# Kernel optimization log

Hardware: AMD Instinct MI355X
Metric: run time of the kernel (lower is better)

The kernel has to match this reference:

```python
import jax, jax.numpy as jnp
import numpy as np

B, C, W, H, K = 8, 512, 64, 64, 64
C4 = C // 4

def setup_inputs() -> dict:
    key = jax.random.key(0)
    ks = jax.random.split(key, 12)
    return {
        "x1": jax.random.normal(ks[0], (B, C, W, H), jnp.float32),
        "y1": jax.random.normal(ks[1], (B, K, C), jnp.float32),
        "x2": jax.random.normal(ks[2], (B, C, W, H), jnp.float32),
        "y2": jax.random.normal(ks[3], (B, K, C), jnp.float32),
        "wq": jax.random.normal(ks[4], (C4, C), jnp.float32) * 0.02,
        "bq": jax.random.normal(ks[5], (C4,), jnp.float32) * 0.02,
        "wk": jax.random.normal(ks[6], (C4, C), jnp.float32) * 0.02,
        "bk": jax.random.normal(ks[7], (C4,), jnp.float32) * 0.02,
        "wv": jax.random.normal(ks[8], (C, C), jnp.float32) * 0.02,
        "bv": jax.random.normal(ks[9], (C,), jnp.float32) * 0.02,
        "scale": jax.random.normal(ks[10], (1,), jnp.float32),
        "scale1": jax.random.normal(ks[11], (1,), jnp.float32),
    }

def reference(x1, y1, x2, y2, wq, bq, wk, bk, wv, bv, scale, scale1):
    b, c, w, h = x1.shape
    k = y1.shape[1]
    n = w * h
    # value projections (nn.Linear: y @ W^T + b), kept as [B, C, K]
    pv1 = jnp.einsum('bkc,dc->bdk', y1, wv) + bv[None, :, None]
    pv2 = jnp.einsum('bkc,dc->bdk', y2, wv) + bv[None, :, None]
    # 1x1 conv query: [B, C4, W, H] -> [B, N, C4]
    q = jnp.einsum('bcwh,dc->bwhd', x2, wq) + bq
    q = q.reshape(b, n, -1)
    # key: [B, K, C4] -> bmm contracts over C4
    kk = jnp.einsum('bkc,dc->bkd', y2, wk) + bk  # [B, K, C4]
    energy = jnp.einsum('bnd,bkd->bnk', q, kk)   # [B, N, K]
    attention = jax.nn.softmax(jnp.abs(energy), axis=-1)
    # out = value [B,C,K] @ attention^T [B,K,N] -> [B,C,N]
    out1 = jnp.einsum('bck,bnk->bcn', pv1, attention).reshape(b, c, w, h)
    out1 = scale[0] * out1 + x1
    out2 = jnp.einsum('bck,bnk->bcn', pv2, attention).reshape(b, c, w, h)
    out2 = scale1[0] * out2 + x2
    return (out1, out2)
```

## Files before the change

### kernel.cpp

```cpp
#include <hip/hip_runtime.h>
#include <math.h>

#define Bn 8
#define Cn 512
#define Kn 64
#define C4n 128
#define Nn 4096

typedef short bf16x8 __attribute__((ext_vector_type(8)));
typedef float f32x4  __attribute__((ext_vector_type(4)));
typedef unsigned short u16;

__device__ __forceinline__ u16 f2bf(float f) {
    union { float f; unsigned u; } v; v.f = f;
    unsigned r = v.u + 0x7FFF + ((v.u >> 16) & 1);
    return (u16)(r >> 16);
}
__device__ __forceinline__ float bf2f(u16 h) {
    union { unsigned u; float f; } v; v.u = ((unsigned)h) << 16;
    return v.f;
}
__device__ __forceinline__ bf16x8 cvt8(const float* p) {
    float4 a = *(const float4*)p;
    float4 b = *(const float4*)(p + 4);
    bf16x8 r;
    r[0] = (short)f2bf(a.x); r[1] = (short)f2bf(a.y);
    r[2] = (short)f2bf(a.z); r[3] = (short)f2bf(a.w);
    r[4] = (short)f2bf(b.x); r[5] = (short)f2bf(b.y);
    r[6] = (short)f2bf(b.z); r[7] = (short)f2bf(b.w);
    return r;
}

__global__ __launch_bounds__(256) void kk_pv_kernel(
    const float* __restrict__ y1, const float* __restrict__ y2,
    const float* __restrict__ wv, const float* __restrict__ bv,
    const float* __restrict__ wk, const float* __restrict__ bk,
    u16* __restrict__ pv1h, u16* __restrict__ pv2h, u16* __restrict__ kkh)
{
    const int b    = blockIdx.y;
    const int sel  = blockIdx.z;
    const int lane = threadIdx.x & 63;
    const int wid  = threadIdx.x >> 6;
    const int lr   = lane & 15;
    const int lg   = lane >> 4;

    if (sel < 2) {
        const int cb   = blockIdx.x * 64 + wid * 16;
        const float* y = sel ? y2 : y1;
        u16* pvh       = sel ? pv2h : pv1h;

        f32x4 acc[4];
        #pragma unroll
        for (int kt = 0; kt < 4; ++kt) acc[kt] = (f32x4){0.f, 0.f, 0.f, 0.f};

        for (int c0 = 0; c0 < Cn; c0 += 32) {
            const int cf = c0 + lg * 8;
            bf16x8 wfr = cvt8(wv + (size_t)(cb + lr) * Cn + cf);
            bf16x8 yfr[4];
            #pragma unroll
            for (int kt = 0; kt < 4; ++kt)
                yfr[kt] = cvt8(y + (size_t)(b * Kn + kt * 16 + lr) * Cn + cf);
            #pragma unroll
            for (int kt = 0; kt < 4; ++kt)
                acc[kt] = __builtin_amdgcn_mfma_f32_16x16x32_bf16(
                    yfr[kt], wfr, acc[kt], 0, 0, 0);
        }
        const int c = cb + lr;
        const float bb = bv[c];
        #pragma unroll
        for (int kt = 0; kt < 4; ++kt) {
            ushort4 o;
            o.x = f2bf(acc[kt][0] + bb); o.y = f2bf(acc[kt][1] + bb);
            o.z = f2bf(acc[kt][2] + bb); o.w = f2bf(acc[kt][3] + bb);
            *(ushort4*)&pvh[(((size_t)(b * Cn + c)) << 6) + kt * 16 + 4 * lg] = o;
        }
    } else {
        const int dblk = blockIdx.x * 16;
        f32x4 acc = (f32x4){0.f, 0.f, 0.f, 0.f};
        for (int c0 = 0; c0 < Cn; c0 += 32) {
            const int cf = c0 + lg * 8;
            bf16x8 wfr = cvt8(wk + (size_t)(dblk + lr) * Cn + cf);
            bf16x8 yfr = cvt8(y2 + (size_t)(b * Kn + wid * 16 + lr) * Cn + cf);
            acc = __builtin_amdgcn_mfma_f32_16x16x32_bf16(wfr, yfr, acc, 0, 0, 0);
        }
        const int d4 = dblk + 4 * lg;
        float4 bkv = *(const float4*)&bk[d4];
        ushort4 o;
        o.x = f2bf(acc[0] + bkv.x); o.y = f2bf(acc[1] + bkv.y);
        o.z = f2bf(acc[2] + bkv.z); o.w = f2bf(acc[3] + bkv.w);
        *(ushort4*)&kkh[(((size_t)(b * Kn + wid * 16 + lr)) << 7) + d4] = o;
    }
}

__global__ __launch_bounds__(256) void M_e0_kernel(
    const u16* __restrict__ kkh, const float* __restrict__ wq,
    const float* __restrict__ bq, u16* __restrict__ Mth,
    float* __restrict__ e0)
{
    const int b = blockIdx.y;
    const int t = threadIdx.x;

    if (blockIdx.x == 4) {
        if (t < Kn) {
            const u16* row = kkh + (((size_t)(b * Kn + t)) << 7);
            float acc = 0.f;
            #pragma unroll
            for (int d8 = 0; d8 < C4n; d8 += 8) {
                bf16x8 v = *(const bf16x8*)(row + d8);
                #pragma unroll
                for (int j = 0; j < 8; ++j)
                    acc += bq[d8 + j] * bf2f((u16)v[j]);
            }
            e0[b * Kn + t] = acc;
        }
        return;
    }

    const int cb   = blockIdx.x * 128 + (t >> 6) * 32;
    const int lane = t & 63;
    const int lr   = lane & 15;
    const int lg   = lane >> 4;

    f32x4 acc[2][4];
    #pragma unroll
    for (int ct = 0; ct < 2; ++ct)
        #pragma unroll
        for (int kt = 0; kt < 4; ++kt) acc[ct][kt] = (f32x4){0.f, 0.f, 0.f, 0.f};

    for (int d0 = 0; d0 < C4n; d0 += 32) {
        const int df = d0 + lg * 8;
        bf16x8 afr[2];
        #pragma unroll
        for (int ct = 0; ct < 2; ++ct) {
            const int c = cb + ct * 16 + lr;
            bf16x8 r;
            #pragma unroll
            for (int j = 0; j < 8; ++j)
                r[j] = (short)f2bf(wq[(size_t)(df + j) * Cn + c]);
            afr[ct] = r;
        }
        bf16x8 bfr[4];
        #pragma unroll
        for (int kt = 0; kt < 4; ++kt)
            bfr[kt] = *(const bf16x8*)&kkh[(((size_t)(b * Kn + kt * 16 + lr)) << 7) + df];
        #pragma unroll
        for (int ct = 0; ct < 2; ++ct)
            #pragma unroll
            for (int kt = 0; kt < 4; ++kt)
                acc[ct][kt] = __builtin_amdgcn_mfma_f32_16x16x32_bf16(
                    afr[ct], bfr[kt], acc[ct][kt], 0, 0, 0);
    }
    #pragma unroll
    for (int ct = 0; ct < 2; ++ct) {
        const int c4 = cb + ct * 16 + 4 * lg;
        #pragma unroll
        for (int kt = 0; kt < 4; ++kt) {
            ushort4 o;
            o.x = f2bf(acc[ct][kt][0]); o.y = f2bf(acc[ct][kt][1]);
            o.z = f2bf(acc[ct][kt][2]); o.w = f2bf(acc[ct][kt][3]);
            *(ushort4*)&Mth[(size_t)(b * Kn + kt * 16 + lr) * Cn + c4] = o;
        }
    }
}

__global__ __launch_bounds__(256) void attn_out_kernel(
    const float* __restrict__ x1, const float* __restrict__ x2,
    const u16* __restrict__ pv1h, const u16* __restrict__ pv2h,
    const u16* __restrict__ Mth, const float* __restrict__ e0,
    const float* __restrict__ scale, const float* __restrict__ scale1,
    float* __restrict__ out1, float* __restrict__ out2)
{
    __shared__ u16   attL[64 * 64];
    __shared__ float T[4][16 * 68];

    const int id   = blockIdx.x;
    const int b    = id & 7;
    const int n0   = (id >> 3) * 64;
    const int t    = threadIdx.x;
    const int lane = t & 63;
    const int wid  = t >> 6;
    const int lr   = lane & 15;
    const int lg   = lane >> 4;
    const int nl   = wid * 16 + lr;

    f32x4 eacc[4];
    #pragma unroll
    for (int kt = 0; kt < 4; ++kt) eacc[kt] = (f32x4){0.f, 0.f, 0.f, 0.f};

    const float* xcol = x2 + (((size_t)b * Cn) << 12) + n0 + nl;
    const u16*   mb   = Mth + ((size_t)b << 15) + (size_t)lr * Cn;

    for (int c0 = 0; c0 < Cn; c0 += 32) {
        const int cf = c0 + lg * 8;
        float xs[8];
        #pragma unroll
        for (int j = 0; j < 8; ++j)
            xs[j] = xcol[((size_t)(cf + j)) << 12];
        bf16x8 xfr;
        #pragma unroll
        for (int j = 0; j < 8; ++j) xfr[j] = (short)f2bf(xs[j]);
        #pragma unroll
        for (int kt = 0; kt < 4; ++kt) {
            bf16x8 av = *(const bf16x8*)(mb + ((size_t)kt << 13) + cf);
            eacc[kt] = __builtin_amdgcn_mfma_f32_16x16x32_bf16(av, xfr, eacc[kt], 0, 0, 0);
        }
    }

    {
        float a[4][4];
        float mx = 0.f;
        #pragma unroll
        for (int kt = 0; kt < 4; ++kt) {
            float4 e0v = *(const float4*)&e0[b * Kn + kt * 16 + lg * 4];
            float er[4] = {e0v.x, e0v.y, e0v.z, e0v.w};
            #pragma unroll
            for (int reg = 0; reg < 4; ++reg) {
                float v = fabsf(eacc[kt][reg] + er[reg]);
                a[kt][reg] = v;
                mx = fmaxf(mx, v);
            }
        }
        mx = fmaxf(mx, __shfl_xor(mx, 16));
        mx = fmaxf(mx, __shfl_xor(mx, 32));
        float s = 0.f;
        #pragma unroll
        for (int kt = 0; kt < 4; ++kt)
            #pragma unroll
            for (int reg = 0; reg < 4; ++reg) {
                a[kt][reg] = __expf(a[kt][reg] - mx);
                s += a[kt][reg];
            }
        s += __shfl_xor(s, 16);
        s += __shfl_xor(s, 32);
        const float inv = 1.0f / s;

        #pragma unroll
        for (int kt = 0; kt < 4; ++kt) {
            ushort4 o;
            o.x = f2bf(a[kt][0] * inv); o.y = f2bf(a[kt][1] * inv);
            o.z = f2bf(a[kt][2] * inv); o.w = f2bf(a[kt][3] * inv);
            const int chunk = (kt * 2 + (lg >> 1)) ^ (nl & 7);
            *(ushort4*)&attL[nl * 64 + chunk * 8 + 4 * (lg & 1)] = o;
        }
    }
    __syncthreads();

    bf16x8 af[4][2];
    #pragma unroll
    for (int nt = 0; nt < 4; ++nt)
        #pragma unroll
        for (int ks = 0; ks < 2; ++ks) {
            const int nn = nt * 16 + lr;
            const int chunk = (ks * 4 + lg) ^ (nn & 7);
            af[nt][ks] = *(const bf16x8*)&attL[nn * 64 + chunk * 8];
        }

    const float sA = scale[0], sB = scale1[0];
    float* Tw = &T[wid][0];

    for (int ct = 0; ct < 8; ++ct) {
        const int wc = ct * 64 + wid * 16;

        const u16* p1 = pv1h + (((size_t)(b * Cn + wc + lr)) << 6) + lg * 8;
        const u16* p2 = pv2h + (((size_t)(b * Cn + wc + lr)) << 6) + lg * 8;
        bf16x8 v1[2], v2[2];
        v1[0] = *(const bf16x8*)p1;  v1[1] = *(const bf16x8*)(p1 + 32);
        v2[0] = *(const bf16x8*)p2;  v2[1] = *(const bf16x8*)(p2 + 32);

        f32x4 acc1[4], acc2[4];
        #pragma unroll
        for (int nt = 0; nt < 4; ++nt) {
            f32x4 z = (f32x4){0.f, 0.f, 0.f, 0.f};
            acc1[nt] = __builtin_amdgcn_mfma_f32_16x16x32_bf16(af[nt][0], v1[0], z, 0, 0, 0);
            acc1[nt] = __builtin_amdgcn_mfma_f32_16x16x32_bf16(af[nt][1], v1[1], acc1[nt], 0, 0, 0);
            acc2[nt] = __builtin_amdgcn_mfma_f32_16x16x32_bf16(af[nt][0], v2[0], z, 0, 0, 0);
            acc2[nt] = __builtin_amdgcn_mfma_f32_16x16x32_bf16(af[nt][1], v2[1], acc2[nt], 0, 0, 0);
        }

        #pragma unroll
        for (int nt = 0; nt < 4; ++nt) {
            float4 v;
            v.x = acc1[nt][0]; v.y = acc1[nt][1];
            v.z = acc1[nt][2]; v.w = acc1[nt][3];
            *(float4*)&Tw[lr * 68 + nt * 16 + 4 * lg] = v;
        }
        #pragma unroll
        for (int r4 = 0; r4 < 4; ++r4) {
            const int rloc = r4 * 4 + lg;
            const size_t row = (((size_t)(b * Cn + wc + rloc)) << 12) + n0 + lr * 4;
            float4 a = *(const float4*)&Tw[rloc * 68 + lr * 4];
            float4 xv = *(const float4*)&x1[row];
            f32x4 o;
            o[0] = sA * a.x + xv.x;  o[1] = sA * a.y + xv.y;
            o[2] = sA * a.z + xv.z;  o[3] = sA * a.w + xv.w;
            __builtin_nontemporal_store(o, (f32x4*)&out1[row]);
        }

        #pragma unroll
        for (int nt = 0; nt < 4; ++nt) {
            float4 v;
            v.x = acc2[nt][0]; v.y = acc2[nt][1];
            v.z = acc2[nt][2]; v.w = acc2[nt][3];
            *(float4*)&Tw[lr * 68 + nt * 16 + 4 * lg] = v;
        }
        #pragma unroll
        for (int r4 = 0; r4 < 4; ++r4) {
            const int rloc = r4 * 4 + lg;
            const size_t row = (((size_t)(b * Cn + wc + rloc)) << 12) + n0 + lr * 4;
            float4 a = *(const float4*)&Tw[rloc * 68 + lr * 4];
            float4 xv = *(const float4*)&x2[row];
            f32x4 o;
            o[0] = sB * a.x + xv.x;  o[1] = sB * a.y + xv.y;
            o[2] = sB * a.z + xv.z;  o[3] = sB * a.w + xv.w;
            __builtin_nontemporal_store(o, (f32x4*)&out2[row]);
        }
    }
}

extern "C" void kernel_launch(void* const* d_in, const int* in_sizes, int n_in,
                              void* d_out, int out_size, void* d_ws, size_t ws_size,
                              hipStream_t stream)
{
    const float* x1     = (const float*)d_in[0];
    const float* y1     = (const float*)d_in[1];
    const float* x2     = (const float*)d_in[2];
    const float* y2     = (const float*)d_in[3];
    const float* wq     = (const float*)d_in[4];
    const float* bq     = (const float*)d_in[5];
    const float* wk     = (const float*)d_in[6];
    const float* bk     = (const float*)d_in[7];
    const float* wv     = (const float*)d_in[8];
    const float* bv     = (const float*)d_in[9];
    const float* scale  = (const float*)d_in[10];
    const float* scale1 = (const float*)d_in[11];

    float* out1 = (float*)d_out;
    float* out2 = out1 + (size_t)Bn * Cn * Nn;

    float* ws   = (float*)d_ws;
    float* e0   = ws;
    u16*   kkh  = (u16*)(ws + 512);
    u16*   Mth  = kkh + 65536;
    u16*   pv1h = Mth + 262144;
    u16*   pv2h = pv1h + 262144;

    kk_pv_kernel<<<dim3(8, Bn, 3), 256, 0, stream>>>(
        y1, y2, wv, bv, wk, bk, pv1h, pv2h, kkh);
    M_e0_kernel<<<dim3(5, Bn), 256, 0, stream>>>(kkh, wq, bq, Mth, e0);
    attn_out_kernel<<<512, 256, 0, stream>>>(
        x1, x2, pv1h, pv2h, Mth, e0, scale, scale1, out1, out2);
}
```

Baseline: 86.04 us.

## Software-pipeline value and residual loads in attention output loop

In the output loop, the pv1/pv2 value fragments and the x1/x2 residual tiles for the next channel tile are now loaded before the current tile's epilogue, so global latency overlaps with the MFMA and LDS work. The attention LDS buffer and the transpose scratch are merged into one shared allocation, with a barrier added once the attention fragments are in registers. Separate scratch regions for out1 and out2 let both epilogues run in a single pass. The cost is higher register pressure from the double-buffered loads, which may reduce occupancy.

```diff
diff --git a/kernel.cpp b/kernel.cpp
--- a/kernel.cpp
+++ b/kernel.cpp
@@ -170,8 +170,8 @@
     const float* __restrict__ scale, const float* __restrict__ scale1,
     float* __restrict__ out1, float* __restrict__ out2)
 {
-    __shared__ u16   attL[64 * 64];
-    __shared__ float T[4][16 * 68];
+    __shared__ float smem[4 * 2176];
+    u16* attL = (u16*)smem;
 
     const int id   = blockIdx.x;
     const int b    = id & 7;
@@ -254,19 +254,28 @@
             const int chunk = (ks * 4 + lg) ^ (nn & 7);
             af[nt][ks] = *(const bf16x8*)&attL[nn * 64 + chunk * 8];
         }
+    __syncthreads();
 
     const float sA = scale[0], sB = scale1[0];
-    float* Tw = &T[wid][0];
+    float* Tw1 = smem + wid * 2176;
+    float* Tw2 = Tw1 + 1088;
+
+    const size_t rowb = (((size_t)(b * Cn + wid * 16 + lg)) << 12) + n0 + lr * 4;
+
+    const u16* p1 = pv1h + (((size_t)(b * Cn + wid * 16 + lr)) << 6) + lg * 8;
+    const u16* p2 = pv2h + (((size_t)(b * Cn + wid * 16 + lr)) << 6) + lg * 8;
+    bf16x8 v1[2], v2[2];
+    v1[0] = *(const bf16x8*)p1;  v1[1] = *(const bf16x8*)(p1 + 32);
+    v2[0] = *(const bf16x8*)p2;  v2[1] = *(const bf16x8*)(p2 + 32);
+    float4 xv1[4], xv2[4];
+    #pragma unroll
+    for (int r4 = 0; r4 < 4; ++r4) {
+        const size_t row = rowb + ((size_t)(r4 * 4) << 12);
+        xv1[r4] = *(const float4*)&x1[row];
+        xv2[r4] = *(const float4*)&x2[row];
+    }
 
     for (int ct = 0; ct < 8; ++ct) {
-        const int wc = ct * 64 + wid * 16;
-
-        const u16* p1 = pv1h + (((size_t)(b * Cn + wc + lr)) << 6) + lg * 8;
-        const u16* p2 = pv2h + (((size_t)(b * Cn + wc + lr)) << 6) + lg * 8;
-        bf16x8 v1[2], v2[2];
-        v1[0] = *(const bf16x8*)p1;  v1[1] = *(const bf16x8*)(p1 + 32);
-        v2[0] = *(const bf16x8*)p2;  v2[1] = *(const bf16x8*)(p2 + 32);
-
         f32x4 acc1[4], acc2[4];
         #pragma unroll
         for (int nt = 0; nt < 4; ++nt) {
@@ -277,43 +286,51 @@
             acc2[nt] = __builtin_amdgcn_mfma_f32_16x16x32_bf16(af[nt][1], v2[1], acc2[nt], 0, 0, 0);
         }
 
+        bf16x8 nv1[2], nv2[2];
+        float4 nx1[4], nx2[4];
+        if (ct < 7) {
+            const int wc = (ct + 1) * 64 + wid * 16;
+            const u16* q1 = pv1h + (((size_t)(b * Cn + wc + lr)) << 6) + lg * 8;
+            const u16* q2 = pv2h + (((size_t)(b * Cn + wc + lr)) << 6) + lg * 8;
+            nv1[0] = *(const bf16x8*)q1;  nv1[1] = *(const bf16x8*)(q1 + 32);
+            nv2[0] = *(const bf16x8*)q2;  nv2[1] = *(const bf16x8*)(q2 + 32);
+            #pragma unroll
+            for (int r4 = 0; r4 < 4; ++r4) {
+                const size_t row = rowb + ((size_t)((ct + 1) * 64 + r4 * 4) << 12);
+                nx1[r4] = *(const float4*)&x1[row];
+                nx2[r4] = *(const float4*)&x2[row];
+            }
+        }
+
         #pragma unroll
         for (int nt = 0; nt < 4; ++nt) {
-            float4 v;
-            v.x = acc1[nt][0]; v.y = acc1[nt][1];
-            v.z = acc1[nt][2]; v.w = acc1[nt][3];
-            *(float4*)&Tw[lr * 68 + nt * 16 + 4 * lg] = v;
+            float4 u, w;
+            u.x = acc1[nt][0]; u.y = acc1[nt][1];
+            u.z = acc1[nt][2]; u.w = acc1[nt][3];
+            w.x = acc2[nt][0]; w.y = acc2[nt][1];
+            w.z = acc2[nt][2]; w.w = acc2[nt][3];
+            *(float4*)&Tw1[lr * 68 + nt * 16 + 4 * lg] = u;
+            *(float4*)&Tw2[lr * 68 + nt * 16 + 4 * lg] = w;
         }
         #pragma unroll
         for (int r4 = 0; r4 < 4; ++r4) {
             const int rloc = r4 * 4 + lg;
-            const size_t row = (((size_t)(b * Cn + wc + rloc)) << 12) + n0 + lr * 4;
-            float4 a = *(const float4*)&Tw[rloc * 68 + lr * 4];
-            float4 xv = *(const float4*)&x1[row];
-            f32x4 o;
-            o[0] = sA * a.x + xv.x;  o[1] = sA * a.y + xv.y;
-            o[2] = sA * a.z + xv.z;  o[3] = sA * a.w + xv.w;
-            __builtin_nontemporal_store(o, (f32x4*)&out1[row]);
-        }
-
-        #pragma unroll
-        for (int nt = 0; nt < 4; ++nt) {
-            float4 v;
-            v.x = acc2[nt][0]; v.y = acc2[nt][1];
-            v.z = acc2[nt][2]; v.w = acc2[nt][3];
-            *(float4*)&Tw[lr * 68 + nt * 16 + 4 * lg] = v;
-        }
-        #pragma unroll
-        for (int r4 = 0; r4 < 4; ++r4) {
-            const int rloc = r4 * 4 + lg;
-            const size_t row = (((size_t)(b * Cn + wc + rloc)) << 12) + n0 + lr * 4;
-            float4 a = *(const float4*)&Tw[rloc * 68 + lr * 4];
-            float4 xv = *(const float4*)&x2[row];
-            f32x4 o;
-            o[0] = sB * a.x + xv.x;  o[1] = sB * a.y + xv.y;
-            o[2] = sB * a.z + xv.z;  o[3] = sB * a.w + xv.w;
-            __builtin_nontemporal_store(o, (f32x4*)&out2[row]);
-        }
+            const size_t row = rowb + ((size_t)(ct * 64 + r4 * 4) << 12);
+            float4 a1 = *(const float4*)&Tw1[rloc * 68 + lr * 4];
+            float4 a2 = *(const float4*)&Tw2[rloc * 68 + lr * 4];
+            f32x4 o1, o2;
+            o1[0] = sA * a1.x + xv1[r4].x;  o1[1] = sA * a1.y + xv1[r4].y;
+            o1[2] = sA * a1.z + xv1[r4].z;  o1[3] = sA * a1.w + xv1[r4].w;
+            o2[0] = sB * a2.x + xv2[r4].x;  o2[1] = sB * a2.y + xv2[r4].y;
+            o2[2] = sB * a2.z + xv2[r4].z;  o2[3] = sB * a2.w + xv2[r4].w;
+            __builtin_nontemporal_store(o1, (f32x4*)&out1[row]);
+            __builtin_nontemporal_store(o2, (f32x4*)&out2[row]);
+        }
+
+        v1[0] = nv1[0]; v1[1] = nv1[1];
+        v2[0] = nv2[0]; v2[1] = nv2[1];
+        #pragma unroll
+        for (int r4 = 0; r4 < 4; ++r4) { xv1[r4] = nx1[r4]; xv2[r4] = nx2[r4]; }
     }
 }
 
```

Result: slower. 93.37 us (+8.5%).

## Fuse key projection and M/e0 computation into projection kernel via LDS

Applied to the files above, without the earlier changes.

Merges the kk projection and the M/e0 kernel into the projection kernel. Each sel==2 block recomputes the full per-batch key matrix (64x128) into shared memory, then computes its 64-column slice of M and, in block 0, e0. This removes one kernel launch and the global round trip for kk, but the key projection is now computed redundantly by 8 blocks per batch, and the wk and y2 reads are repeated per block.

```diff
diff --git a/kernel.cpp b/kernel.cpp
--- a/kernel.cpp
+++ b/kernel.cpp
@@ -31,12 +31,16 @@
     return r;
 }
 
-__global__ __launch_bounds__(256) void kk_pv_kernel(
+__global__ __launch_bounds__(256) void proj_kernel(
     const float* __restrict__ y1, const float* __restrict__ y2,
     const float* __restrict__ wv, const float* __restrict__ bv,
     const float* __restrict__ wk, const float* __restrict__ bk,
-    u16* __restrict__ pv1h, u16* __restrict__ pv2h, u16* __restrict__ kkh)
+    const float* __restrict__ wq, const float* __restrict__ bq,
+    u16* __restrict__ pv1h, u16* __restrict__ pv2h,
+    u16* __restrict__ Mth, float* __restrict__ e0)
 {
+    __shared__ u16 kkL[64 * 136];
+
     const int b    = blockIdx.y;
     const int sel  = blockIdx.z;
     const int lane = threadIdx.x & 63;
@@ -74,91 +78,65 @@
             o.z = f2bf(acc[kt][2] + bb); o.w = f2bf(acc[kt][3] + bb);
             *(ushort4*)&pvh[(((size_t)(b * Cn + c)) << 6) + kt * 16 + 4 * lg] = o;
         }
-    } else {
-        const int dblk = blockIdx.x * 16;
+        return;
+    }
+
+    const int kt = wid;
+
+    bf16x8 yfr[16];
+    #pragma unroll
+    for (int cc = 0; cc < 16; ++cc)
+        yfr[cc] = cvt8(y2 + (size_t)(b * Kn + kt * 16 + lr) * Cn + cc * 32 + lg * 8);
+
+    for (int dt = 0; dt < 8; ++dt) {
         f32x4 acc = (f32x4){0.f, 0.f, 0.f, 0.f};
-        for (int c0 = 0; c0 < Cn; c0 += 32) {
-            const int cf = c0 + lg * 8;
-            bf16x8 wfr = cvt8(wk + (size_t)(dblk + lr) * Cn + cf);
-            bf16x8 yfr = cvt8(y2 + (size_t)(b * Kn + wid * 16 + lr) * Cn + cf);
-            acc = __builtin_amdgcn_mfma_f32_16x16x32_bf16(wfr, yfr, acc, 0, 0, 0);
-        }
-        const int d4 = dblk + 4 * lg;
+        #pragma unroll
+        for (int cc = 0; cc < 16; ++cc) {
+            bf16x8 wfr = cvt8(wk + (size_t)(dt * 16 + lr) * Cn + cc * 32 + lg * 8);
+            acc = __builtin_amdgcn_mfma_f32_16x16x32_bf16(wfr, yfr[cc], acc, 0, 0, 0);
+        }
+        const int d4 = dt * 16 + 4 * lg;
         float4 bkv = *(const float4*)&bk[d4];
         ushort4 o;
         o.x = f2bf(acc[0] + bkv.x); o.y = f2bf(acc[1] + bkv.y);
         o.z = f2bf(acc[2] + bkv.z); o.w = f2bf(acc[3] + bkv.w);
-        *(ushort4*)&kkh[(((size_t)(b * Kn + wid * 16 + lr)) << 7) + d4] = o;
-    }
-}
-
-__global__ __launch_bounds__(256) void M_e0_kernel(
-    const u16* __restrict__ kkh, const float* __restrict__ wq,
-    const float* __restrict__ bq, u16* __restrict__ Mth,
-    float* __restrict__ e0)
-{
-    const int b = blockIdx.y;
-    const int t = threadIdx.x;
-
-    if (blockIdx.x == 4) {
-        if (t < Kn) {
-            const u16* row = kkh + (((size_t)(b * Kn + t)) << 7);
-            float acc = 0.f;
-            #pragma unroll
-            for (int d8 = 0; d8 < C4n; d8 += 8) {
-                bf16x8 v = *(const bf16x8*)(row + d8);
-                #pragma unroll
-                for (int j = 0; j < 8; ++j)
-                    acc += bq[d8 + j] * bf2f((u16)v[j]);
+        *(ushort4*)&kkL[(kt * 16 + lr) * 136 + d4] = o;
+    }
+    __syncthreads();
+
+    if (blockIdx.x == 0 && threadIdx.x < Kn) {
+        const int k = threadIdx.x;
+        float acc = 0.f;
+        #pragma unroll 16
+        for (int d = 0; d < C4n; ++d)
+            acc += bq[d] * bf2f(kkL[k * 136 + d]);
+        e0[b * Kn + k] = acc;
+    }
+
+    {
+        const int cb = blockIdx.x * 64 + wid * 16;
+        f32x4 acc[4];
+        #pragma unroll
+        for (int q = 0; q < 4; ++q) acc[q] = (f32x4){0.f, 0.f, 0.f, 0.f};
+
+        for (int d0 = 0; d0 < C4n; d0 += 32) {
+            const int df = d0 + lg * 8;
+            bf16x8 afr;
+            #pragma unroll
+            for (int j = 0; j < 8; ++j)
+                afr[j] = (short)f2bf(wq[(size_t)(df + j) * Cn + cb + lr]);
+            #pragma unroll
+            for (int q = 0; q < 4; ++q) {
+                bf16x8 bfr = *(const bf16x8*)&kkL[(q * 16 + lr) * 136 + df];
+                acc[q] = __builtin_amdgcn_mfma_f32_16x16x32_bf16(afr, bfr, acc[q], 0, 0, 0);
             }
-            e0[b * Kn + t] = acc;
-        }
-        return;
-    }
-
-    const int cb   = blockIdx.x * 128 + (t >> 6) * 32;
-    const int lane = t & 63;
-    const int lr   = lane & 15;
-    const int lg   = lane >> 4;
-
-    f32x4 acc[2][4];
-    #pragma unroll
-    for (int ct = 0; ct < 2; ++ct)
-        #pragma unroll
-        for (int kt = 0; kt < 4; ++kt) acc[ct][kt] = (f32x4){0.f, 0.f, 0.f, 0.f};
-
-    for (int d0 = 0; d0 < C4n; d0 += 32) {
-        const int df = d0 + lg * 8;
-        bf16x8 afr[2];
-        #pragma unroll
-        for (int ct = 0; ct < 2; ++ct) {
-            const int c = cb + ct * 16 + lr;
-            bf16x8 r;
-            #pragma unroll
-            for (int j = 0; j < 8; ++j)
-                r[j] = (short)f2bf(wq[(size_t)(df + j) * Cn + c]);
-            afr[ct] = r;
-        }
-        bf16x8 bfr[4];
-        #pragma unroll
-        for (int kt = 0; kt < 4; ++kt)
-            bfr[kt] = *(const bf16x8*)&kkh[(((size_t)(b * Kn + kt * 16 + lr)) << 7) + df];
-        #pragma unroll
-        for (int ct = 0; ct < 2; ++ct)
-            #pragma unroll
-            for (int kt = 0; kt < 4; ++kt)
-                acc[ct][kt] = __builtin_amdgcn_mfma_f32_16x16x32_bf16(
-                    afr[ct], bfr[kt], acc[ct][kt], 0, 0, 0);
-    }
-    #pragma unroll
-    for (int ct = 0; ct < 2; ++ct) {
-        const int c4 = cb + ct * 16 + 4 * lg;
-        #pragma unroll
-        for (int kt = 0; kt < 4; ++kt) {
+        }
+        #pragma unroll
+        for (int q = 0; q < 4; ++q) {
             ushort4 o;
-            o.x = f2bf(acc[ct][kt][0]); o.y = f2bf(acc[ct][kt][1]);
-            o.z = f2bf(acc[ct][kt][2]); o.w = f2bf(acc[ct][kt][3]);
-            *(ushort4*)&Mth[(size_t)(b * Kn + kt * 16 + lr) * Cn + c4] = o;
+            o.x = f2bf(acc[q][0]); o.y = f2bf(acc[q][1]);
+            o.z = f2bf(acc[q][2]); o.w = f2bf(acc[q][3]);
+            *(ushort4*)&Mth[(size_t)(b * Kn + q * 16 + lr) * Cn + cb + 4 * lg] = o;
         }
     }
 }
@@ -339,14 +317,12 @@
 
     float* ws   = (float*)d_ws;
     float* e0   = ws;
-    u16*   kkh  = (u16*)(ws + 512);
-    u16*   Mth  = kkh + 65536;
+    u16*   Mth  = (u16*)(ws + 512);
     u16*   pv1h = Mth + 262144;
     u16*   pv2h = pv1h + 262144;
 
-    kk_pv_kernel<<<dim3(8, Bn, 3), 256, 0, stream>>>(
-        y1, y2, wv, bv, wk, bk, pv1h, pv2h, kkh);
-    M_e0_kernel<<<dim3(5, Bn), 256, 0, stream>>>(kkh, wq, bq, Mth, e0);
+    proj_kernel<<<dim3(8, Bn, 3), 256, 0, stream>>>(
+        y1, y2, wv, bv, wk, bk, wq, bq, pv1h, pv2h, Mth, e0);
     attn_out_kernel<<<512, 256, 0, stream>>>(
         x1, x2, pv1h, pv2h, Mth, e0, scale, scale1, out1, out2);
 }
```

Measured after the change: 120.2 us. 39.8% more time.
